# Kernel tuning notes

Measured on AMD Instinct MI355X. Metric: run time of the kernel, lower is better.

## Reference

```python
import jax, jax.numpy as jnp
import numpy as np

N_VARS = 8
D_MODEL = 512
L = 8192
B = 32
G = 1  # num_global_tokens
PATCH_LENS = [16, 16, 32, 32, 64, 64, 128, 128]
SAMPLING = [1, 1, 2, 2, 1, 1, 2, 2]
UNIQUE_PLS = [16, 32, 64, 128]


def _pos_emb(n, d):
    # standard sinusoidal positional embedding (Informer/Transformer style)
    pos = np.arange(n, dtype=np.float32)[:, None]
    div = np.exp(np.arange(0, d, 2, dtype=np.float32) * (-np.log(10000.0) / d))
    pe = np.zeros((n, d), dtype=np.float32)
    pe[:, 0::2] = np.sin(pos * div)
    pe[:, 1::2] = np.cos(pos * div)
    return jnp.asarray(pe)


def setup_inputs() -> dict:
    key = jax.random.key(0)
    ks = jax.random.split(key, 16)
    inp = {"x": jax.random.normal(ks[0], (B, N_VARS, L), dtype=jnp.float32)}
    # one Linear(patch_len, d_model) per unique patch_len; torch Linear weight is (out,in)
    for i, pl in enumerate(UNIQUE_PLS):
        bound = 1.0 / np.sqrt(pl)
        inp[f"w{pl}"] = jax.random.uniform(ks[1 + 2 * i], (D_MODEL, pl), minval=-bound, maxval=bound, dtype=jnp.float32)
        inp[f"b{pl}"] = jax.random.uniform(ks[2 + 2 * i], (D_MODEL,), minval=-bound, maxval=bound, dtype=jnp.float32)
    inp["glb_tokens"] = jax.random.normal(ks[10], (1, G, D_MODEL), dtype=jnp.float32)
    inp["channel_emb"] = jax.random.normal(ks[11], (N_VARS, D_MODEL), dtype=jnp.float32)
    return inp


def reference(x, w16, b16, w32, b32, w64, b64, w128, b128, glb_tokens, channel_emb):
    wdict = {16: (w16, b16), 32: (w32, b32), 64: (w64, b64), 128: (w128, b128)}
    Bn = x.shape[0]
    min_sp = min(SAMPLING)
    outs = []
    for v in range(N_VARS):
        pl = PATCH_LENS[v]
        sf = SAMPLING[v] // min_sp
        n_p = L // (pl * sf)  # num patches for this variable
        # strided gather: element j of patch i sits at i*pl*sf + j*sf -> reshape trick
        patches = x[:, v, : n_p * pl * sf].reshape(Bn, n_p, pl, sf)[..., 0]  # [B, n_p, pl]
        w, b = wdict[pl]
        emb = jnp.einsum('bnp,dp->bnd', patches, w) + b          # [B, n_p, d]
        emb = emb + _pos_emb(n_p, D_MODEL)                        # positional add
        emb = jnp.concatenate([emb, jnp.broadcast_to(glb_tokens, (Bn, G, D_MODEL))], axis=1)
        emb = emb + channel_emb[v]                                # channel add (incl. global token)
        outs.append(emb)
    return jnp.concatenate(outs, axis=1)  # [B, sum(n_p + G), d] = [32, 1608, 512]
```

## Files before the change

kernel.cpp:

```cpp
#include <hip/hip_runtime.h>
#include <math.h>

#define DM 512
#define LSEQ 8192
#define NV 8
#define TOK 1608
#define BROWS 32
#define NTHR 256

typedef _Float16 h2 __attribute__((ext_vector_type(2)));
typedef float f4n __attribute__((ext_vector_type(4)));

__device__ __constant__ int c_segv[8]   = {6, 7, 4, 5, 2, 3, 0, 1};
__device__ __constant__ int c_cum[9]    = {0, 64, 128, 384, 640, 896, 1152, 2176, 3200};
__device__ __constant__ int c_lgch[8]   = {0, 0, 2, 2, 2, 2, 4, 4};
__device__ __constant__ int c_tokoff[8] = {0, 513, 1026, 1155, 1284, 1413, 1542, 1575};
__device__ __constant__ int c_np[8]     = {512, 512, 128, 128, 128, 128, 32, 32};
__device__ __constant__ int c_pl[8]     = {16, 16, 32, 32, 64, 64, 128, 128};
__device__ __constant__ int c_sf[8]     = {1, 1, 2, 2, 1, 1, 2, 2};
__device__ __constant__ int c_wtoff[8]  = {262144, 262144, 266240, 266240,
                                           274432, 274432, 290816, 290816};

__device__ __forceinline__ float fdot2f(h2 a, h2 b, float c) {
#if __has_builtin(__builtin_amdgcn_fdot2)
    return __builtin_amdgcn_fdot2(a, b, c, false);
#else
    return fmaf((float)a.y, (float)b.y, fmaf((float)a.x, (float)b.x, c));
#endif
}
__device__ __forceinline__ h2 bch2(unsigned u) { return __builtin_bit_cast(h2, u); }

__device__ __forceinline__ void nt_store4(float* p, float4 v) {
#if __has_builtin(__builtin_nontemporal_store)
    f4n t; t.x = v.x; t.y = v.y; t.z = v.z; t.w = v.w;
    __builtin_nontemporal_store(t, reinterpret_cast<f4n*>(p));
#else
    *reinterpret_cast<float4*>(p) = v;
#endif
}

__global__ __launch_bounds__(512) void setup_kernel(
    const float* __restrict__ w16, const float* __restrict__ w32,
    const float* __restrict__ w64, const float* __restrict__ w128,
    float* __restrict__ ws)
{
    int bid = blockIdx.x;
    int d = threadIdx.x;
    if (bid < 512) {
        int idx = bid * 512 + d;
        int i = idx >> 9;
        int dd = idx & (DM - 1);
        const float c = -9.210340371976184f / 512.0f;
        float div = expf((float)(dd & ~1) * c);
        float ang = (float)i * div;
        ws[idx] = (dd & 1) ? cosf(ang) : sinf(ang);
        return;
    }
    int j = bid - 512;
    const float* w; int pl, k2, off;
    if (j < 8)       { w = w16;  pl = 16;  k2 = j;      off = 262144; }
    else if (j < 24) { w = w32;  pl = 32;  k2 = j - 8;  off = 266240; }
    else if (j < 56) { w = w64;  pl = 64;  k2 = j - 24; off = 274432; }
    else             { w = w128; pl = 128; k2 = j - 56; off = 290816; }
    float2 p = *reinterpret_cast<const float2*>(w + (size_t)d * pl + 2 * k2);
    h2 h; h.x = (_Float16)p.x; h.y = (_Float16)p.y;
    reinterpret_cast<unsigned*>(ws)[off + k2 * DM + d] = __builtin_bit_cast(unsigned, h);
}

__global__ __launch_bounds__(NTHR, 5) void patch_embed_kernel(
    const float* __restrict__ x,
    const float* __restrict__ b16,  const float* __restrict__ b32,
    const float* __restrict__ b64,  const float* __restrict__ b128,
    const float* __restrict__ glb,  const float* __restrict__ chan,
    const float* __restrict__ ws,   float* __restrict__ out)
{
    extern __shared__ float ldsf[];
    unsigned* ldsu = reinterpret_cast<unsigned*>(ldsf);
    int bid = blockIdx.x;
    const int tid = threadIdx.x;

    if (bid >= 3200) {
        int v = bid - 3200;
        int d2 = tid << 1;
        float2 g = *reinterpret_cast<const float2*>(glb + d2);
        float2 c = *reinterpret_cast<const float2*>(chan + v * DM + d2);
        float2 o; o.x = g.x + c.x; o.y = g.y + c.y;
        int row0 = c_tokoff[v] + c_np[v];
        for (int b = 0; b < 32; ++b)
            *reinterpret_cast<float2*>(out + ((size_t)(b * TOK + row0)) * DM + d2) = o;
        return;
    }

    int seg = 0;
    while (bid >= c_cum[seg + 1]) ++seg;
    int local = bid - c_cum[seg];
    int v = c_segv[seg];
    int h = local & 1;
    int rest = local >> 1;
    int lg = c_lgch[seg];
    int b = rest >> lg;
    int chunk = rest & ((1 << lg) - 1);
    const int pl = c_pl[v];
    const int sf = c_sf[v];
    const int pl2 = pl >> 1;
    const int i0 = chunk * BROWS;

    const int ne2 = (BROWS * pl) >> 1;
    const float* xb = x + ((size_t)b * NV + v) * LSEQ + (size_t)i0 * (pl * sf);
    if (sf == 1) {
        for (int t = tid; t < (ne2 >> 1); t += NTHR) {
            float4 q = *reinterpret_cast<const float4*>(xb + 4 * t);
            h2 a; a.x = (_Float16)q.x; a.y = (_Float16)q.y;
            h2 c; c.x = (_Float16)q.z; c.y = (_Float16)q.w;
            uint2 o; o.x = __builtin_bit_cast(unsigned, a);
            o.y = __builtin_bit_cast(unsigned, c);
            *reinterpret_cast<uint2*>(ldsu + 2 * t) = o;
        }
    } else {
        for (int p = tid; p < ne2; p += NTHR) {
            float4 q = *reinterpret_cast<const float4*>(xb + 4 * p);
            h2 a; a.x = (_Float16)q.x; a.y = (_Float16)q.z;
            ldsu[p] = __builtin_bit_cast(unsigned, a);
        }
    }
    __syncthreads();

    const int lane = tid & 63;
    const int wv   = tid >> 6;
    const int c0   = (h << 8) + (lane << 2);
    const unsigned* prow = ldsu + (wv * 8) * pl2;
    const unsigned* wtv  = reinterpret_cast<const unsigned*>(ws) + c_wtoff[v];

    float acc[8][4];
#pragma unroll
    for (int r = 0; r < 8; ++r)
#pragma unroll
        for (int c = 0; c < 4; ++c) acc[r][c] = 0.f;

    uint4 w0 = *reinterpret_cast<const uint4*>(wtv + c0);
    uint4 w1 = *reinterpret_cast<const uint4*>(wtv + DM + c0);

    for (int k2 = 0; k2 < pl2; k2 += 2) {
        uint4 n0, n1;
        if (k2 + 2 < pl2) {
            const unsigned* wn = wtv + (k2 + 2) * DM;
            n0 = *reinterpret_cast<const uint4*>(wn + c0);
            n1 = *reinterpret_cast<const uint4*>(wn + DM + c0);
        }
        uint2 pr[8];
#pragma unroll
        for (int r = 0; r < 8; ++r)
            pr[r] = *reinterpret_cast<const uint2*>(prow + r * pl2 + k2);
#pragma unroll
        for (int r = 0; r < 8; ++r) {
            h2 p0 = bch2(pr[r].x);
            h2 p1 = bch2(pr[r].y);
            acc[r][0] = fdot2f(p1, bch2(w1.x), fdot2f(p0, bch2(w0.x), acc[r][0]));
            acc[r][1] = fdot2f(p1, bch2(w1.y), fdot2f(p0, bch2(w0.y), acc[r][1]));
            acc[r][2] = fdot2f(p1, bch2(w1.z), fdot2f(p0, bch2(w0.z), acc[r][2]));
            acc[r][3] = fdot2f(p1, bch2(w1.w), fdot2f(p0, bch2(w0.w), acc[r][3]));
        }
        w0 = n0; w1 = n1;
    }

    const float* bias = (pl == 16) ? b16 : (pl == 32) ? b32 : (pl == 64) ? b64 : b128;
    float4 bc;
    {
        float4 ba = *reinterpret_cast<const float4*>(bias + c0);
        float4 ca = *reinterpret_cast<const float4*>(chan + v * DM + c0);
        bc.x = ba.x + ca.x; bc.y = ba.y + ca.y;
        bc.z = ba.z + ca.z; bc.w = ba.w + ca.w;
    }

    const int row0 = i0 + wv * 8;
    float* ob = out + ((size_t)(b * TOK + c_tokoff[v] + row0)) * DM + c0;
    const float* pb = ws  + (size_t)row0 * DM + c0;
#pragma unroll
    for (int r = 0; r < 8; ++r) {
        float4 pA = *reinterpret_cast<const float4*>(pb + (size_t)r * DM);
        float4 o;
        o.x = acc[r][0] + bc.x + pA.x;
        o.y = acc[r][1] + bc.y + pA.y;
        o.z = acc[r][2] + bc.z + pA.z;
        o.w = acc[r][3] + bc.w + pA.w;
        nt_store4(ob + (size_t)r * DM, o);
    }
}

extern "C" void kernel_launch(void* const* d_in, const int* in_sizes, int n_in,
                              void* d_out, int out_size, void* d_ws, size_t ws_size,
                              hipStream_t stream) {
    const float* x    = (const float*)d_in[0];
    const float* w16  = (const float*)d_in[1];
    const float* b16  = (const float*)d_in[2];
    const float* w32  = (const float*)d_in[3];
    const float* b32  = (const float*)d_in[4];
    const float* w64  = (const float*)d_in[5];
    const float* b64  = (const float*)d_in[6];
    const float* w128 = (const float*)d_in[7];
    const float* b128 = (const float*)d_in[8];
    const float* glb  = (const float*)d_in[9];
    const float* chan = (const float*)d_in[10];
    float* out = (float*)d_out;
    float* ws  = (float*)d_ws;

    hipLaunchKernelGGL(setup_kernel, dim3(632), dim3(512), 0, stream,
                       w16, w32, w64, w128, ws);
    hipLaunchKernelGGL(patch_embed_kernel, dim3(3208), dim3(NTHR),
                       BROWS * 64 * sizeof(unsigned),
                       stream,
                       x, b16, b32, b64, b128, glb, chan, ws, out);
}
```

Baseline: 37.85 us.

## Read patches directly from global memory with wave-uniform addresses, drop LDS staging

Removes the LDS staging of the x patches and the block barrier. Each wave now loads its eight patch rows straight from global memory with a wave-uniform (readfirstlane) base address, so the loads can become scalar or broadcast reads, and converts them to fp16 with packed round-toward-zero conversions. The setup kernel switches to fast-math exp, sin and cos intrinsics for the positional table. The trade-offs are redundant x loads across the two column-half blocks and within each wave, slightly different rounding in the fp16 conversion, and lower accuracy in the sinusoidal table.

New measurement: 50.06 us. +32.2%, slower.

```diff
diff --git a/kernel.cpp b/kernel.cpp
--- a/kernel.cpp
+++ b/kernel.cpp
@@ -29,6 +29,14 @@
 #endif
 }
 __device__ __forceinline__ h2 bch2(unsigned u) { return __builtin_bit_cast(h2, u); }
+
+__device__ __forceinline__ h2 pkrtz(float a, float b) {
+#if __has_builtin(__builtin_amdgcn_cvt_pkrtz)
+    return __builtin_bit_cast(h2, __builtin_amdgcn_cvt_pkrtz(a, b));
+#else
+    h2 r; r.x = (_Float16)a; r.y = (_Float16)b; return r;
+#endif
+}
 
 __device__ __forceinline__ void nt_store4(float* p, float4 v) {
 #if __has_builtin(__builtin_nontemporal_store)
@@ -51,9 +59,9 @@
         int i = idx >> 9;
         int dd = idx & (DM - 1);
         const float c = -9.210340371976184f / 512.0f;
-        float div = expf((float)(dd & ~1) * c);
+        float div = __expf((float)(dd & ~1) * c);
         float ang = (float)i * div;
-        ws[idx] = (dd & 1) ? cosf(ang) : sinf(ang);
+        ws[idx] = (dd & 1) ? __cosf(ang) : __sinf(ang);
         return;
     }
     int j = bid - 512;
@@ -67,6 +75,12 @@
     reinterpret_cast<unsigned*>(ws)[off + k2 * DM + d] = __builtin_bit_cast(unsigned, h);
 }
 
+#define DOT4(r, P, X)                                           \
+    acc[r][0] = fdot2f(P, bch2((X).x), acc[r][0]);              \
+    acc[r][1] = fdot2f(P, bch2((X).y), acc[r][1]);              \
+    acc[r][2] = fdot2f(P, bch2((X).z), acc[r][2]);              \
+    acc[r][3] = fdot2f(P, bch2((X).w), acc[r][3]);
+
 __global__ __launch_bounds__(NTHR, 5) void patch_embed_kernel(
     const float* __restrict__ x,
     const float* __restrict__ b16,  const float* __restrict__ b32,
@@ -74,8 +88,6 @@
     const float* __restrict__ glb,  const float* __restrict__ chan,
     const float* __restrict__ ws,   float* __restrict__ out)
 {
-    extern __shared__ float ldsf[];
-    unsigned* ldsu = reinterpret_cast<unsigned*>(ldsf);
     int bid = blockIdx.x;
     const int tid = threadIdx.x;
 
@@ -105,31 +117,13 @@
     const int pl2 = pl >> 1;
     const int i0 = chunk * BROWS;
 
-    const int ne2 = (BROWS * pl) >> 1;
-    const float* xb = x + ((size_t)b * NV + v) * LSEQ + (size_t)i0 * (pl * sf);
-    if (sf == 1) {
-        for (int t = tid; t < (ne2 >> 1); t += NTHR) {
-            float4 q = *reinterpret_cast<const float4*>(xb + 4 * t);
-            h2 a; a.x = (_Float16)q.x; a.y = (_Float16)q.y;
-            h2 c; c.x = (_Float16)q.z; c.y = (_Float16)q.w;
-            uint2 o; o.x = __builtin_bit_cast(unsigned, a);
-            o.y = __builtin_bit_cast(unsigned, c);
-            *reinterpret_cast<uint2*>(ldsu + 2 * t) = o;
-        }
-    } else {
-        for (int p = tid; p < ne2; p += NTHR) {
-            float4 q = *reinterpret_cast<const float4*>(xb + 4 * p);
-            h2 a; a.x = (_Float16)q.x; a.y = (_Float16)q.z;
-            ldsu[p] = __builtin_bit_cast(unsigned, a);
-        }
-    }
-    __syncthreads();
-
     const int lane = tid & 63;
-    const int wv   = tid >> 6;
+    const int wvu  = __builtin_amdgcn_readfirstlane(tid >> 6);
     const int c0   = (h << 8) + (lane << 2);
-    const unsigned* prow = ldsu + (wv * 8) * pl2;
-    const unsigned* wtv  = reinterpret_cast<const unsigned*>(ws) + c_wtoff[v];
+
+    const float* prow_g = x + ((size_t)b * NV + v) * LSEQ
+                            + (size_t)(i0 + wvu * 8) * (pl * sf);
+    const unsigned* wtv = reinterpret_cast<const unsigned*>(ws) + c_wtoff[v];
 
     float acc[8][4];
 #pragma unroll
@@ -143,22 +137,32 @@
     for (int k2 = 0; k2 < pl2; k2 += 2) {
         uint4 n0, n1;
         if (k2 + 2 < pl2) {
-            const unsigned* wn = wtv + (k2 + 2) * DM;
+            const unsigned* wn = wtv + (size_t)(k2 + 2) * DM;
             n0 = *reinterpret_cast<const uint4*>(wn + c0);
             n1 = *reinterpret_cast<const uint4*>(wn + DM + c0);
         }
-        uint2 pr[8];
-#pragma unroll
-        for (int r = 0; r < 8; ++r)
-            pr[r] = *reinterpret_cast<const uint2*>(prow + r * pl2 + k2);
+        h2 p0[8], p1[8];
+        if (sf == 1) {
+#pragma unroll
+            for (int r = 0; r < 8; ++r) {
+                f4n q = *reinterpret_cast<const f4n*>(prow_g + r * pl + 2 * k2);
+                p0[r] = pkrtz(q.x, q.y);
+                p1[r] = pkrtz(q.z, q.w);
+            }
+        } else {
+#pragma unroll
+            for (int r = 0; r < 8; ++r) {
+                const float* pb_ = prow_g + r * (pl << 1) + (k2 << 2);
+                f4n qa = *reinterpret_cast<const f4n*>(pb_);
+                f4n qb = *reinterpret_cast<const f4n*>(pb_ + 4);
+                p0[r] = pkrtz(qa.x, qa.z);
+                p1[r] = pkrtz(qb.x, qb.z);
+            }
+        }
 #pragma unroll
         for (int r = 0; r < 8; ++r) {
-            h2 p0 = bch2(pr[r].x);
-            h2 p1 = bch2(pr[r].y);
-            acc[r][0] = fdot2f(p1, bch2(w1.x), fdot2f(p0, bch2(w0.x), acc[r][0]));
-            acc[r][1] = fdot2f(p1, bch2(w1.y), fdot2f(p0, bch2(w0.y), acc[r][1]));
-            acc[r][2] = fdot2f(p1, bch2(w1.z), fdot2f(p0, bch2(w0.z), acc[r][2]));
-            acc[r][3] = fdot2f(p1, bch2(w1.w), fdot2f(p0, bch2(w0.w), acc[r][3]));
+            DOT4(r, p0[r], w0)
+            DOT4(r, p1[r], w1)
         }
         w0 = n0; w1 = n1;
     }
@@ -172,7 +176,7 @@
         bc.z = ba.z + ca.z; bc.w = ba.w + ca.w;
     }
 
-    const int row0 = i0 + wv * 8;
+    const int row0 = i0 + wvu * 8;
     float* ob = out + ((size_t)(b * TOK + c_tokoff[v] + row0)) * DM + c0;
     const float* pb = ws  + (size_t)row0 * DM + c0;
 #pragma unroll
@@ -206,8 +210,6 @@
 
     hipLaunchKernelGGL(setup_kernel, dim3(632), dim3(512), 0, stream,
                        w16, w32, w64, w128, ws);
-    hipLaunchKernelGGL(patch_embed_kernel, dim3(3208), dim3(NTHR),
-                       BROWS * 64 * sizeof(unsigned),
-                       stream,
+    hipLaunchKernelGGL(patch_embed_kernel, dim3(3208), dim3(NTHR), 0, stream,
                        x, b16, b32, b64, b128, glb, chan, ws, out);
 }
```

## Compute positional embedding inline with fast sin/cos instead of a precomputed table

Applied to the files above, without the earlier changes.

The setup kernel no longer builds a 512x512 sinusoidal table in workspace. The main kernel now computes each positional value in its epilogue with __expf/__sinf/__cosf. This removes 512 setup blocks and a 1 MB table read per output tile in exchange for transcendental ALU work and lower precision from the fast intrinsics at large angles. It also raises the occupancy hint from 5 to 6 and splits the fdot2 chains per k-pair.

New measurement: 37.86 us. No clear change (+0.0%).

```diff
diff --git a/kernel.cpp b/kernel.cpp
--- a/kernel.cpp
+++ b/kernel.cpp
@@ -18,8 +18,7 @@
 __device__ __constant__ int c_np[8]     = {512, 512, 128, 128, 128, 128, 32, 32};
 __device__ __constant__ int c_pl[8]     = {16, 16, 32, 32, 64, 64, 128, 128};
 __device__ __constant__ int c_sf[8]     = {1, 1, 2, 2, 1, 1, 2, 2};
-__device__ __constant__ int c_wtoff[8]  = {262144, 262144, 266240, 266240,
-                                           274432, 274432, 290816, 290816};
+__device__ __constant__ int c_wtoff[8]  = {0, 0, 4096, 4096, 12288, 12288, 28672, 28672};
 
 __device__ __forceinline__ float fdot2f(h2 a, h2 b, float c) {
 #if __has_builtin(__builtin_amdgcn_fdot2)
@@ -44,30 +43,25 @@
     const float* __restrict__ w64, const float* __restrict__ w128,
     float* __restrict__ ws)
 {
-    int bid = blockIdx.x;
+    int j = blockIdx.x;
     int d = threadIdx.x;
-    if (bid < 512) {
-        int idx = bid * 512 + d;
-        int i = idx >> 9;
-        int dd = idx & (DM - 1);
-        const float c = -9.210340371976184f / 512.0f;
-        float div = expf((float)(dd & ~1) * c);
-        float ang = (float)i * div;
-        ws[idx] = (dd & 1) ? cosf(ang) : sinf(ang);
-        return;
-    }
-    int j = bid - 512;
     const float* w; int pl, k2, off;
-    if (j < 8)       { w = w16;  pl = 16;  k2 = j;      off = 262144; }
-    else if (j < 24) { w = w32;  pl = 32;  k2 = j - 8;  off = 266240; }
-    else if (j < 56) { w = w64;  pl = 64;  k2 = j - 24; off = 274432; }
-    else             { w = w128; pl = 128; k2 = j - 56; off = 290816; }
+    if (j < 8)       { w = w16;  pl = 16;  k2 = j;      off = 0; }
+    else if (j < 24) { w = w32;  pl = 32;  k2 = j - 8;  off = 4096; }
+    else if (j < 56) { w = w64;  pl = 64;  k2 = j - 24; off = 12288; }
+    else             { w = w128; pl = 128; k2 = j - 56; off = 28672; }
     float2 p = *reinterpret_cast<const float2*>(w + (size_t)d * pl + 2 * k2);
     h2 h; h.x = (_Float16)p.x; h.y = (_Float16)p.y;
     reinterpret_cast<unsigned*>(ws)[off + k2 * DM + d] = __builtin_bit_cast(unsigned, h);
 }
 
-__global__ __launch_bounds__(NTHR, 5) void patch_embed_kernel(
+#define DOT4(r, P, X)                                           \
+    acc[r][0] = fdot2f(P, bch2((X).x), acc[r][0]);              \
+    acc[r][1] = fdot2f(P, bch2((X).y), acc[r][1]);              \
+    acc[r][2] = fdot2f(P, bch2((X).z), acc[r][2]);              \
+    acc[r][3] = fdot2f(P, bch2((X).w), acc[r][3]);
+
+__global__ __launch_bounds__(NTHR, 6) void patch_embed_kernel(
     const float* __restrict__ x,
     const float* __restrict__ b16,  const float* __restrict__ b32,
     const float* __restrict__ b64,  const float* __restrict__ b128,
@@ -143,7 +137,7 @@
     for (int k2 = 0; k2 < pl2; k2 += 2) {
         uint4 n0, n1;
         if (k2 + 2 < pl2) {
-            const unsigned* wn = wtv + (k2 + 2) * DM;
+            const unsigned* wn = wtv + (size_t)(k2 + 2) * DM;
             n0 = *reinterpret_cast<const uint4*>(wn + c0);
             n1 = *reinterpret_cast<const uint4*>(wn + DM + c0);
         }
@@ -153,12 +147,8 @@
             pr[r] = *reinterpret_cast<const uint2*>(prow + r * pl2 + k2);
 #pragma unroll
         for (int r = 0; r < 8; ++r) {
-            h2 p0 = bch2(pr[r].x);
-            h2 p1 = bch2(pr[r].y);
-            acc[r][0] = fdot2f(p1, bch2(w1.x), fdot2f(p0, bch2(w0.x), acc[r][0]));
-            acc[r][1] = fdot2f(p1, bch2(w1.y), fdot2f(p0, bch2(w0.y), acc[r][1]));
-            acc[r][2] = fdot2f(p1, bch2(w1.z), fdot2f(p0, bch2(w0.z), acc[r][2]));
-            acc[r][3] = fdot2f(p1, bch2(w1.w), fdot2f(p0, bch2(w0.w), acc[r][3]));
+            DOT4(r, bch2(pr[r].x), w0)
+            DOT4(r, bch2(pr[r].y), w1)
         }
         w0 = n0; w1 = n1;
     }
@@ -172,17 +162,22 @@
         bc.z = ba.z + ca.z; bc.w = ba.w + ca.w;
     }
 
+    const float kc_ = -9.210340371976184f / 512.0f;
+    const float div0 = __expf((float)c0 * kc_);
+    const float div2 = __expf((float)(c0 + 2) * kc_);
+
     const int row0 = i0 + wv * 8;
     float* ob = out + ((size_t)(b * TOK + c_tokoff[v] + row0)) * DM + c0;
-    const float* pb = ws  + (size_t)row0 * DM + c0;
 #pragma unroll
     for (int r = 0; r < 8; ++r) {
-        float4 pA = *reinterpret_cast<const float4*>(pb + (size_t)r * DM);
+        float fi = (float)(row0 + r);
+        float a0 = fi * div0;
+        float a2 = fi * div2;
         float4 o;
-        o.x = acc[r][0] + bc.x + pA.x;
-        o.y = acc[r][1] + bc.y + pA.y;
-        o.z = acc[r][2] + bc.z + pA.z;
-        o.w = acc[r][3] + bc.w + pA.w;
+        o.x = acc[r][0] + bc.x + __sinf(a0);
+        o.y = acc[r][1] + bc.y + __cosf(a0);
+        o.z = acc[r][2] + bc.z + __sinf(a2);
+        o.w = acc[r][3] + bc.w + __cosf(a2);
         nt_store4(ob + (size_t)r * DM, o);
     }
 }
@@ -204,7 +199,7 @@
     float* out = (float*)d_out;
     float* ws  = (float*)d_ws;
 
-    hipLaunchKernelGGL(setup_kernel, dim3(632), dim3(512), 0, stream,
+    hipLaunchKernelGGL(setup_kernel, dim3(120), dim3(512), 0, stream,
                        w16, w32, w64, w128, ws);
     hipLaunchKernelGGL(patch_embed_kernel, dim3(3208), dim3(NTHR),
                        BROWS * 64 * sizeof(unsigned),
```
